# Kernel optimization log

Hardware: AMD Instinct MI355X
Metric: run time of the kernel (lower is better)

## Reference

```python
import jax, jax.numpy as jnp
import numpy as np

B, L, ENC, D, H, HD, MLP, R = 4, 512, 512, 1024, 16, 64, 4096, 32
NUM_BUCKETS, MAX_DISTANCE = 32, 128
EPS = 1e-6
NEG = -1e10


def rmsnorm(x, scale):
    var = jnp.mean(jnp.square(x), axis=-1, keepdims=True)
    return x * jax.lax.rsqrt(var + EPS) * scale


def rel_pos_bias(table, qlen, klen):
    # T5 causal (bidirectional=False) relative position bucketing.
    ctx = jnp.arange(qlen)[:, None]
    mem = jnp.arange(klen)[None, :]
    rp = mem - ctx                      # [q, k]
    n = -jnp.minimum(rp, 0)             # distance into the past
    max_exact = NUM_BUCKETS // 2
    is_small = n < max_exact
    large = max_exact + (
        jnp.log(jnp.maximum(n, 1).astype(jnp.float32) / max_exact)
        / np.log(MAX_DISTANCE / max_exact) * (NUM_BUCKETS - max_exact)
    ).astype(jnp.int32)
    large = jnp.minimum(large, NUM_BUCKETS - 1)
    bucket = jnp.where(is_small, n, large)
    return table[bucket].transpose(2, 0, 1)[None]  # [1, h, q, k]


def lora_dense(x, W, a, b):
    # x:[B,L,d]  W:[d,e]  a:[B,d,r]  b:[B,r,e]  -> xW + (xa)b per example
    out = jnp.einsum('bld,de->ble', x, W)
    low = jnp.einsum('bld,bdr->blr', x, a)
    return out + jnp.einsum('blr,bre->ble', low, b)


def attention(xq, xkv, Wq, Wk, Wv, Wo, qa, qb, ka, kb, va, vb, oa, ob, bias):
    b, ql, _ = xq.shape
    kl = xkv.shape[1]
    q = lora_dense(xq, Wq, qa, qb).reshape(b, ql, H, HD) * (1.0 / np.sqrt(HD))
    k = lora_dense(xkv, Wk, ka, kb).reshape(b, kl, H, HD)
    v = lora_dense(xkv, Wv, va, vb).reshape(b, kl, H, HD)
    scores = jnp.einsum('bqhd,bkhd->bhqk', q, k)
    if bias is not None:
        scores = scores + bias
    probs = jax.nn.softmax(scores, axis=-1)
    ctx = jnp.einsum('bhqk,bkhd->bqhd', probs, v).reshape(b, ql, H * HD)
    return lora_dense(ctx, Wo, oa, ob)


def setup_inputs() -> dict:
    key = jax.random.key(0)
    ks = jax.random.split(key, 32)
    s = 0.02
    inp = {
        'inputs':  jax.random.normal(ks[0], (B, L, D), jnp.float32),
        'encoded': jax.random.normal(ks[1], (B, ENC, D), jnp.float32),
        'lora_qa': jax.random.normal(ks[2], (B, 2, D, R), jnp.float32) * s,
        'lora_qb': jax.random.normal(ks[3], (B, 2, R, D), jnp.float32) * s,
        'lora_ka': jax.random.normal(ks[4], (B, 2, D, R), jnp.float32) * s,
        'lora_kb': jax.random.normal(ks[5], (B, 2, R, D), jnp.float32) * s,
        'lora_va': jax.random.normal(ks[6], (B, 2, D, R), jnp.float32) * s,
        'lora_vb': jax.random.normal(ks[7], (B, 2, R, D), jnp.float32) * s,
        'lora_oa': jax.random.normal(ks[8], (B, 2, D, R), jnp.float32) * s,
        'lora_ob': jax.random.normal(ks[9], (B, 2, R, D), jnp.float32) * s,
        'rel_table': jax.random.normal(ks[10], (NUM_BUCKETS, H), jnp.float32) * s,
        'ln1': jnp.ones((D,), jnp.float32),
        'ln2': jnp.ones((D,), jnp.float32),
        'ln3': jnp.ones((D,), jnp.float32),
        'sWq': jax.random.normal(ks[11], (D, H * HD), jnp.float32) * s,
        'sWk': jax.random.normal(ks[12], (D, H * HD), jnp.float32) * s,
        'sWv': jax.random.normal(ks[13], (D, H * HD), jnp.float32) * s,
        'sWo': jax.random.normal(ks[14], (H * HD, D), jnp.float32) * s,
        'cWq': jax.random.normal(ks[15], (D, H * HD), jnp.float32) * s,
        'cWk': jax.random.normal(ks[16], (D, H * HD), jnp.float32) * s,
        'cWv': jax.random.normal(ks[17], (D, H * HD), jnp.float32) * s,
        'cWo': jax.random.normal(ks[18], (H * HD, D), jnp.float32) * s,
        'wi0': jax.random.normal(ks[19], (D, MLP), jnp.float32) * s,
        'wi1': jax.random.normal(ks[20], (D, MLP), jnp.float32) * s,
        'wo_mlp': jax.random.normal(ks[21], (MLP, D), jnp.float32) * s,
    }
    return inp


def reference(inputs, encoded, lora_qa, lora_qb, lora_ka, lora_kb, lora_va, lora_vb,
              lora_oa, lora_ob, rel_table, ln1, ln2, ln3,
              sWq, sWk, sWv, sWo, cWq, cWk, cWv, cWo, wi0, wi1, wo_mlp):
    l = inputs.shape[1]
    causal = jnp.tril(jnp.ones((l, l), dtype=bool))
    dec_bias = rel_pos_bias(rel_table, l, l) + jnp.where(causal, 0.0, NEG)[None, None]

    # --- self-attention block ---
    x = rmsnorm(inputs, ln1)
    x = attention(x, x, sWq, sWk, sWv, sWo,
                  lora_qa[:, 0], lora_qb[:, 0], lora_ka[:, 0], lora_kb[:, 0],
                  lora_va[:, 0], lora_vb[:, 0], lora_oa[:, 0], lora_ob[:, 0],
                  dec_bias)
    x = x + inputs

    # --- cross-attention block ---
    y = rmsnorm(x, ln2)
    y = attention(y, encoded, cWq, cWk, cWv, cWo,
                  lora_qa[:, 1], lora_qb[:, 1], lora_ka[:, 1], lora_kb[:, 1],
                  lora_va[:, 1], lora_vb[:, 1], lora_oa[:, 1], lora_ob[:, 1],
                  None)
    y = y + x

    # --- gated-gelu MLP block (T5 v1.1 style) ---
    lz = rmsnorm(y, ln3)
    h = jax.nn.gelu(lz @ wi0, approximate=False) * (lz @ wi1)
    z = h @ wo_mlp + y
    return z
```

## Files before the change

### kernel.cpp

```cpp
#include <hip/hip_runtime.h>
#include <math.h>


#define DEV __device__ __forceinline__

typedef __bf16 bf16x8 __attribute__((ext_vector_type(8)));
typedef float floatx4 __attribute__((ext_vector_type(4)));

typedef __attribute__((address_space(1))) void* gas_ptr;
typedef __attribute__((address_space(3))) void* las_ptr;

DEV unsigned short f2bf(float f) {
  union { float f; unsigned int u; } v; v.f = f;
  unsigned int r = v.u + 0x7fffu + ((v.u >> 16) & 1u);
  return (unsigned short)(r >> 16);
}
DEV float bf2f(unsigned short u) {
  union { unsigned int u; float f; } v; v.u = ((unsigned int)u) << 16;
  return v.f;
}

#define GLOAD_LDS16(g, l) __builtin_amdgcn_global_load_lds((gas_ptr)(g), (las_ptr)(l), 16, 0, 0)

template<int NW>
DEV void stage_tile_sw(const char* gbase, char* lds, int nrows, int ldbytes, int wave, int lane) {
  int nchunks = nrows >> 3;
  int colb = (((lane & 7) ^ ((lane >> 3) & 7)) << 4);
  for (int c = wave; c < nchunks; c += NW) {
    int row = (c << 3) + (lane >> 3);
    GLOAD_LDS16(gbase + (size_t)row * ldbytes + colb, lds + (c << 10));
  }
}

template<int NW>
DEV void stage_tile256_sw(const char* gbase, char* lds, int nrows, int ldbytes, int wave, int lane) {
  int nchunks = nrows >> 2;
  for (int c = wave; c < nchunks; c += NW) {
    int row = (c << 2) + (lane >> 4);
    int key = row & 7;
    int colb = ((lane & 15) ^ key) << 4;
    GLOAD_LDS16(gbase + (size_t)row * ldbytes + colb, lds + (c << 10));
  }
}

template<int WM, int WN>
DEV void gemm_core(const unsigned short* A, const unsigned short* Bt, float* C,
                   int K, int lda, int ldb, int ldc, int m0, int n0,
                   char* ldsA, char* ldsB) {
  constexpr int NW = WM * WN;
  const int tid  = threadIdx.x;
  const int lane = tid & 63;
  const int wave = tid >> 6;
  const int wm   = wave % WM;
  const int wn   = wave / WM;
  const int quad = lane >> 4;
  const int l15  = lane & 15;
  const int key  = l15 & 7;

  floatx4 acc[4][4];
#pragma unroll
  for (int i = 0; i < 4; ++i)
#pragma unroll
    for (int j = 0; j < 4; ++j) acc[i][j] = (floatx4){0.f, 0.f, 0.f, 0.f};

  const char* gA = (const char*)(A + (size_t)m0 * lda);
  const char* gB = (const char*)(Bt + (size_t)n0 * ldb);

  for (int k0 = 0; k0 < K; k0 += 64) {
    stage_tile_sw<NW>(gA + (size_t)k0 * 2, ldsA, WM * 64, lda * 2, wave, lane);
    stage_tile_sw<NW>(gB + (size_t)k0 * 2, ldsB, WN * 64, ldb * 2, wave, lane);
    __syncthreads();
#pragma unroll
    for (int kk = 0; kk < 64; kk += 32) {
      bf16x8 af[4], bv[4];
      int off = (((kk >> 3) + quad) ^ key) << 4;
      const char* baseA = ldsA + (size_t)(wm * 64 + l15) * 128 + off;
      const char* baseB = ldsB + (size_t)(wn * 64 + l15) * 128 + off;
#pragma unroll
      for (int mi = 0; mi < 4; ++mi) af[mi] = *(const bf16x8*)(baseA + mi * 2048);
#pragma unroll
      for (int ni = 0; ni < 4; ++ni) bv[ni] = *(const bf16x8*)(baseB + ni * 2048);
#pragma unroll
      for (int mi = 0; mi < 4; ++mi)
#pragma unroll
        for (int ni = 0; ni < 4; ++ni)
          acc[mi][ni] = __builtin_amdgcn_mfma_f32_16x16x32_bf16(af[mi], bv[ni], acc[mi][ni], 0, 0, 0);
    }
    __syncthreads();
  }

#pragma unroll
  for (int mi = 0; mi < 4; ++mi) {
#pragma unroll
    for (int r = 0; r < 4; ++r) {
      int row = m0 + wm * 64 + mi * 16 + quad * 4 + r;
#pragma unroll
      for (int ni = 0; ni < 4; ++ni) {
        int col = n0 + wn * 64 + ni * 16 + l15;
        C[(size_t)row * ldc + col] = acc[mi][ni][r];
      }
    }
  }
}

__global__ __launch_bounds__(256) void k_gemm1s(const unsigned short* A, const unsigned short* Bt,
                                                float* Cpart, size_t pstride,
                                                int Kchunk, int lda, int ldb, int ldc) {
  __shared__ char lds[32768];
  int s = blockIdx.z;
  size_t koff = (size_t)s * Kchunk;
  gemm_core<2, 2>(A + koff, Bt + koff, Cpart + (size_t)s * pstride,
                  Kchunk, lda, ldb, ldc,
                  blockIdx.y * 128, blockIdx.x * 128, lds, lds + 16384);
}

struct GXSlice {
  const unsigned short* A0;
  const unsigned short* Aext;
  const unsigned short* B0;
  const unsigned short* Bext;
  float* C;
  size_t bextb;
  int ldc, nxa, it0, it1;
};
struct GX { GXSlice s[4]; };

__global__ __launch_bounds__(256) void k_gemmx(GX g) {
  __shared__ char lds[32768];
  char* ldsA = lds;
  char* ldsB = lds + 16384;
  GXSlice sl = g.s[blockIdx.z];
  if ((int)blockIdx.x >= sl.nxa) return;
  const int m0 = blockIdx.y * 128, n0 = blockIdx.x * 128;
  const int b = m0 >> 9;
  const int tid = threadIdx.x, lane = tid & 63, wave = tid >> 6;
  const int wm = wave & 1, wn = wave >> 1;
  const int quad = lane >> 4, l15 = lane & 15;
  const int key = l15 & 7;

  floatx4 acc[4][4];
#pragma unroll
  for (int i = 0; i < 4; ++i)
#pragma unroll
    for (int j = 0; j < 4; ++j) acc[i][j] = (floatx4){0.f, 0.f, 0.f, 0.f};

  for (int it = sl.it0; it < sl.it1; ++it) {
    if (it < 16) {
      stage_tile_sw<4>((const char*)sl.A0 + (size_t)m0 * 2048 + it * 128, ldsA, 128, 2048, wave, lane);
      stage_tile_sw<4>((const char*)sl.B0 + (size_t)n0 * 2048 + it * 128, ldsB, 128, 2048, wave, lane);
    } else {
      int eb = (it - 16) * 128;
      stage_tile_sw<4>((const char*)sl.Aext + (size_t)m0 * 256 + eb, ldsA, 128, 256, wave, lane);
      stage_tile_sw<4>((const char*)(sl.Bext + (size_t)b * sl.bextb) + (size_t)n0 * 256 + eb,
                       ldsB, 128, 256, wave, lane);
    }
    __syncthreads();
#pragma unroll
    for (int kk = 0; kk < 64; kk += 32) {
      bf16x8 af[4], bv[4];
      int off = (((kk >> 3) + quad) ^ key) << 4;
      const char* baseA = ldsA + (size_t)(wm * 64 + l15) * 128 + off;
      const char* baseB = ldsB + (size_t)(wn * 64 + l15) * 128 + off;
#pragma unroll
      for (int mi = 0; mi < 4; ++mi) af[mi] = *(const bf16x8*)(baseA + mi * 2048);
#pragma unroll
      for (int ni = 0; ni < 4; ++ni) bv[ni] = *(const bf16x8*)(baseB + ni * 2048);
#pragma unroll
      for (int mi = 0; mi < 4; ++mi)
#pragma unroll
        for (int ni = 0; ni < 4; ++ni)
          acc[mi][ni] = __builtin_amdgcn_mfma_f32_16x16x32_bf16(af[mi], bv[ni], acc[mi][ni], 0, 0, 0);
    }
    __syncthreads();
  }

#pragma unroll
  for (int mi = 0; mi < 4; ++mi) {
#pragma unroll
    for (int r = 0; r < 4; ++r) {
      int row = m0 + wm * 64 + mi * 16 + quad * 4 + r;
#pragma unroll
      for (int ni = 0; ni < 4; ++ni) {
        int col = n0 + wn * 64 + ni * 16 + l15;
        sl.C[(size_t)row * sl.ldc + col] = acc[mi][ni][r];
      }
    }
  }
}

struct QKVSlice {
  const unsigned short* A0;
  const unsigned short* Aext;
  const unsigned short* B0;
  const unsigned short* Bext;
  unsigned short* sec0;
  unsigned short* sec1;
  unsigned short* sec2;
  size_t bextb;
  int vsec, nxa;
};
struct QKV2 { QKVSlice s[2]; };

__global__ __launch_bounds__(256) void k_gemmqkv(QKV2 g) {
  __shared__ char lds[34816];
  char* ldsA = lds;
  char* ldsB = lds + 16384;
  QKVSlice sl = g.s[blockIdx.z];
  if ((int)blockIdx.x >= sl.nxa) return;
  const int m0 = blockIdx.y * 128, n0 = blockIdx.x * 128;
  const int b = m0 >> 9;
  const int tid = threadIdx.x, lane = tid & 63, wave = tid >> 6;
  const int wm = wave & 1, wn = wave >> 1;
  const int quad = lane >> 4, l15 = lane & 15;
  const int key = l15 & 7;

  floatx4 acc[4][4];
#pragma unroll
  for (int i = 0; i < 4; ++i)
#pragma unroll
    for (int j = 0; j < 4; ++j) acc[i][j] = (floatx4){0.f, 0.f, 0.f, 0.f};

  for (int it = 0; it < 18; ++it) {
    if (it < 16) {
      stage_tile_sw<4>((const char*)sl.A0 + (size_t)m0 * 2048 + it * 128, ldsA, 128, 2048, wave, lane);
      stage_tile_sw<4>((const char*)sl.B0 + (size_t)n0 * 2048 + it * 128, ldsB, 128, 2048, wave, lane);
    } else {
      int eb = (it - 16) * 128;
      stage_tile_sw<4>((const char*)sl.Aext + (size_t)m0 * 256 + eb, ldsA, 128, 256, wave, lane);
      stage_tile_sw<4>((const char*)(sl.Bext + (size_t)b * sl.bextb) + (size_t)n0 * 256 + eb,
                       ldsB, 128, 256, wave, lane);
    }
    __syncthreads();
#pragma unroll
    for (int kk = 0; kk < 64; kk += 32) {
      bf16x8 af[4], bv[4];
      int off = (((kk >> 3) + quad) ^ key) << 4;
      const char* baseA = ldsA + (size_t)(wm * 64 + l15) * 128 + off;
      const char* baseB = ldsB + (size_t)(wn * 64 + l15) * 128 + off;
#pragma unroll
      for (int mi = 0; mi < 4; ++mi) af[mi] = *(const bf16x8*)(baseA + mi * 2048);
#pragma unroll
      for (int ni = 0; ni < 4; ++ni) bv[ni] = *(const bf16x8*)(baseB + ni * 2048);
#pragma unroll
      for (int mi = 0; mi < 4; ++mi)
#pragma unroll
        for (int ni = 0; ni < 4; ++ni)
          acc[mi][ni] = __builtin_amdgcn_mfma_f32_16x16x32_bf16(af[mi], bv[ni], acc[mi][ni], 0, 0, 0);
    }
    __syncthreads();
  }

  const int sec = n0 >> 10;
  const int nloc = n0 & 1023;
  if (sec != sl.vsec) {
    unsigned short* dst = (sec == 0) ? sl.sec0 : sl.sec1;
#pragma unroll
    for (int mi = 0; mi < 4; ++mi)
#pragma unroll
      for (int r = 0; r < 4; ++r) {
        int row = m0 + wm * 64 + mi * 16 + quad * 4 + r;
        unsigned short* drow = dst + (size_t)row * 1024 + nloc + wn * 64;
#pragma unroll
        for (int ni = 0; ni < 4; ++ni)
          drow[ni * 16 + l15] = f2bf(acc[mi][ni][r]);
      }
  } else {
    unsigned short* vdstb = (sl.vsec == 1) ? sl.sec1 : sl.sec2;
    char* vbuf = lds + (size_t)(wm * 2 + wn) * 8704;
#pragma unroll
    for (int ni = 0; ni < 4; ++ni)
#pragma unroll
      for (int mi = 0; mi < 4; ++mi) {
        unsigned long long pk =
            (unsigned long long)f2bf(acc[mi][ni][0])
          | ((unsigned long long)f2bf(acc[mi][ni][1]) << 16)
          | ((unsigned long long)f2bf(acc[mi][ni][2]) << 32)
          | ((unsigned long long)f2bf(acc[mi][ni][3]) << 48);
        *(unsigned long long*)(vbuf + (size_t)(ni * 16 + l15) * 136 + (mi * 16 + quad * 4) * 2) = pk;
      }
    __syncthreads();
    int dbase = nloc + wn * 64;
    int h = dbase >> 6;
    int kb = (m0 & 511) + wm * 64;
    unsigned short* vdst = vdstb + (size_t)(b * 16 + h) * 64 * 512;
    int lh = lane >> 3, ll = lane & 7;
#pragma unroll
    for (int i = 0; i < 8; ++i) {
      int d = i * 8 + lh;
      const char* p = vbuf + (size_t)d * 136 + ll * 16;
      unsigned long long lo = *(const unsigned long long*)p;
      unsigned long long hi = *(const unsigned long long*)(p + 8);
      uint4 v;
      v.x = (unsigned)lo; v.y = (unsigned)(lo >> 32);
      v.z = (unsigned)hi; v.w = (unsigned)(hi >> 32);
      *(uint4*)(vdst + (size_t)d * 512 + kb + ll * 8) = v;
    }
  }
}

template<bool CAUSAL, bool QSUM>
__global__ __launch_bounds__(256) void k_flash(const unsigned short* qmat, const float* qparts,
                                               const unsigned short* kmat, const unsigned short* vt,
                                               const float* rb, unsigned short* ctxb) {
  __shared__ char ldsQ[8192];
  __shared__ char ldsK[16384];
  __shared__ char ldsV[16384];
  __shared__ char ldsP[16384];
  __shared__ float lrb[512];

  const size_t PART = (size_t)2048 * 1024;
  const int z = blockIdx.y, b = z >> 4, h = z & 15;
  const int q0 = blockIdx.x * 64;
  const int tid = threadIdx.x, lane = tid & 63, wave = tid >> 6;
  const int quad = lane >> 4, l15 = lane & 15;
  const int key = l15 & 7;

  const unsigned short* K = kmat + (size_t)b * 512 * 1024 + h * 64;
  const unsigned short* V = vt + (size_t)z * 64 * 512;

  if (QSUM) {
#pragma unroll
    for (int rr = 0; rr < 4; ++rr) {
      int row = rr * 16 + (tid >> 4);
      int c4 = tid & 15;
      const float* src = qparts + (size_t)(q0 + row) * 1024 + h * 64 + c4 * 4;
      float4 s0 = *(const float4*)src;
      float4 s1 = *(const float4*)(src + PART);
      float4 s2 = *(const float4*)(src + 2 * PART);
      float4 s3 = *(const float4*)(src + 3 * PART);
      ushort4 o;
      o.x = f2bf(s0.x + s1.x + s2.x + s3.x);
      o.y = f2bf(s0.y + s1.y + s2.y + s3.y);
      o.z = f2bf(s0.z + s1.z + s2.z + s3.z);
      o.w = f2bf(s0.w + s1.w + s2.w + s3.w);
      int qoff = (((c4 >> 1) ^ (row & 7)) << 4) | ((c4 & 1) << 3);
      *(ushort4*)(ldsQ + (size_t)row * 128 + qoff) = o;
    }
  } else {
    const unsigned short* Q = qmat + (size_t)b * 512 * 1024 + h * 64;
    stage_tile_sw<4>((const char*)(Q + (size_t)q0 * 1024), ldsQ, 64, 2048, wave, lane);
  }
  if (CAUSAL)
    for (int i = tid; i < 512; i += 256) lrb[i] = rb[h * 512 + i];

  float m_run[4], l_run[4];
  floatx4 oacc[4];
#pragma unroll
  for (int r = 0; r < 4; ++r) { m_run[r] = -1e30f; l_run[r] = 0.f; }
#pragma unroll
  for (int ni = 0; ni < 4; ++ni) oacc[ni] = (floatx4){0.f, 0.f, 0.f, 0.f};

  const int ktend = CAUSAL ? (blockIdx.x / 2 + 1) : 4;
  for (int kt = 0; kt < ktend; ++kt) {
    __syncthreads();
    stage_tile_sw<4>((const char*)(K + (size_t)kt * 128 * 1024), ldsK, 128, 2048, wave, lane);
    stage_tile256_sw<4>((const char*)(V + kt * 128), ldsV, 64, 1024, wave, lane);
    __syncthreads();

    floatx4 sacc[8];
#pragma unroll
    for (int ct = 0; ct < 8; ++ct) sacc[ct] = (floatx4){0.f, 0.f, 0.f, 0.f};
    const size_t qrow = (size_t)(wave * 16 + l15) * 128;
#pragma unroll
    for (int kd = 0; kd < 2; ++kd) {
      int offq = ((quad + kd * 4) ^ key) << 4;
      bf16x8 af = *(const bf16x8*)(ldsQ + qrow + offq);
#pragma unroll
      for (int ct = 0; ct < 8; ++ct) {
        bf16x8 bfv = *(const bf16x8*)(ldsK + (size_t)(ct * 16 + l15) * 128 + offq);
        sacc[ct] = __builtin_amdgcn_mfma_f32_16x16x32_bf16(af, bfv, sacc[ct], 0, 0, 0);
      }
    }

    float sv[8][4];
#pragma unroll
    for (int ct = 0; ct < 8; ++ct)
#pragma unroll
      for (int r = 0; r < 4; ++r) {
        float v = sacc[ct][r] * 0.125f;
        if (CAUSAL) {
          int qq = q0 + wave * 16 + quad * 4 + r;
          int kk = kt * 128 + ct * 16 + l15;
          v = (kk <= qq) ? v + lrb[qq - kk] : -1e30f;
        }
        sv[ct][r] = v;
      }

    float mx[4];
#pragma unroll
    for (int r = 0; r < 4; ++r) {
      mx[r] = sv[0][r];
#pragma unroll
      for (int ct = 1; ct < 8; ++ct) mx[r] = fmaxf(mx[r], sv[ct][r]);
    }
#pragma unroll
    for (int o = 1; o < 16; o <<= 1)
#pragma unroll
      for (int r = 0; r < 4; ++r) mx[r] = fmaxf(mx[r], __shfl_xor(mx[r], o));

    float alpha[4], rs[4];
#pragma unroll
    for (int r = 0; r < 4; ++r) {
      float mn = fmaxf(m_run[r], mx[r]);
      alpha[r] = __expf(m_run[r] - mn);
      m_run[r] = mn;
      rs[r] = 0.f;
    }
#pragma unroll
    for (int ct = 0; ct < 8; ++ct)
#pragma unroll
      for (int r = 0; r < 4; ++r) {
        float p = __expf(sv[ct][r] - m_run[r]);
        sv[ct][r] = p;
        rs[r] += p;
      }
#pragma unroll
    for (int o = 1; o < 16; o <<= 1)
#pragma unroll
      for (int r = 0; r < 4; ++r) rs[r] += __shfl_xor(rs[r], o);
#pragma unroll
    for (int r = 0; r < 4; ++r) l_run[r] = l_run[r] * alpha[r] + rs[r];
#pragma unroll
    for (int ni = 0; ni < 4; ++ni)
#pragma unroll
      for (int r = 0; r < 4; ++r) oacc[ni][r] *= alpha[r];

#pragma unroll
    for (int ct = 0; ct < 8; ++ct)
#pragma unroll
      for (int r = 0; r < 4; ++r) {
        int prow_w = wave * 16 + quad * 4 + r;
        int kidx = ct * 16 + l15;
        int pb = (((kidx >> 3) ^ (prow_w & 7)) << 4) | ((kidx & 7) << 1);
        *(unsigned short*)(ldsP + (size_t)prow_w * 256 + pb) = f2bf(sv[ct][r]);
      }
    __syncthreads();

    const size_t prow = (size_t)(wave * 16 + l15) * 256;
#pragma unroll
    for (int kk = 0; kk < 4; ++kk) {
      int offp = ((quad + kk * 4) ^ key) << 4;
      bf16x8 pf = *(const bf16x8*)(ldsP + prow + offp);
#pragma unroll
      for (int ni = 0; ni < 4; ++ni) {
        bf16x8 vf8 = *(const bf16x8*)(ldsV + (size_t)(ni * 16 + l15) * 256 + offp);
        oacc[ni] = __builtin_amdgcn_mfma_f32_16x16x32_bf16(pf, vf8, oacc[ni], 0, 0, 0);
      }
    }
  }

#pragma unroll
  for (int r = 0; r < 4; ++r) {
    int q = q0 + wave * 16 + quad * 4 + r;
    float inv = 1.0f / l_run[r];
    unsigned short* dst = ctxb + ((size_t)b * 512 + q) * 1024 + h * 64;
#pragma unroll
    for (int ni = 0; ni < 4; ++ni)
      dst[ni * 16 + l15] = f2bf(oacc[ni][r] * inv);
  }
}

__global__ __launch_bounds__(512) void k_mlp(const unsigned short* A, const unsigned short* Wc,
                                             unsigned short* hbf) {
  __shared__ char lds[49152];
  char* ldsA = lds;
  char* ldsB = lds + 16384;
  const int m0 = blockIdx.y * 128;
  const int n0 = blockIdx.x * 128;
  const int tid = threadIdx.x, lane = tid & 63, wave = tid >> 6;
  const int half = wave >> 2, wl = wave & 3;
  const int wm = wl & 1, wn = wl >> 1;
  const int quad = lane >> 4, l15 = lane & 15;
  const int key = l15 & 7;

  floatx4 acc[4][4];
#pragma unroll
  for (int i = 0; i < 4; ++i)
#pragma unroll
    for (int j = 0; j < 4; ++j) acc[i][j] = (floatx4){0.f, 0.f, 0.f, 0.f};

  const char* gA = (const char*)(A + (size_t)m0 * 1024);
  const char* gB = (const char*)(Wc + (size_t)blockIdx.x * 256 * 1024);

  for (int k0 = 0; k0 < 1024; k0 += 64) {
    stage_tile_sw<8>(gA + (size_t)k0 * 2, ldsA, 128, 2048, wave, lane);
    stage_tile_sw<8>(gB + (size_t)k0 * 2, ldsB, 256, 2048, wave, lane);
    __syncthreads();
#pragma unroll
    for (int kk = 0; kk < 64; kk += 32) {
      bf16x8 af[4], bv[4];
      int off = (((kk >> 3) + quad) ^ key) << 4;
      const char* baseA = ldsA + (size_t)(wm * 64 + l15) * 128 + off;
      const char* baseB = ldsB + (size_t)(half * 128 + wn * 64 + l15) * 128 + off;
#pragma unroll
      for (int mi = 0; mi < 4; ++mi) af[mi] = *(const bf16x8*)(baseA + mi * 2048);
#pragma unroll
      for (int ni = 0; ni < 4; ++ni) bv[ni] = *(const bf16x8*)(baseB + ni * 2048);
#pragma unroll
      for (int mi = 0; mi < 4; ++mi)
#pragma unroll
        for (int ni = 0; ni < 4; ++ni)
          acc[mi][ni] = __builtin_amdgcn_mfma_f32_16x16x32_bf16(af[mi], bv[ni], acc[mi][ni], 0, 0, 0);
    }
    __syncthreads();
  }

  if (half == 1) {
#pragma unroll
    for (int mi = 0; mi < 4; ++mi)
#pragma unroll
      for (int r = 0; r < 4; ++r) {
        int row = wm * 64 + mi * 16 + quad * 4 + r;
#pragma unroll
        for (int ni = 0; ni < 4; ++ni) {
          int col = wn * 64 + ni * 16 + l15;
          *(unsigned short*)(ldsB + (size_t)row * 256 + col * 2) = f2bf(acc[mi][ni][r]);
        }
      }
  }
  __syncthreads();
  if (half == 0) {
#pragma unroll
    for (int mi = 0; mi < 4; ++mi)
#pragma unroll
      for (int r = 0; r < 4; ++r) {
        int row = wm * 64 + mi * 16 + quad * 4 + r;
#pragma unroll
        for (int ni = 0; ni < 4; ++ni) {
          int col = wn * 64 + ni * 16 + l15;
          float h1 = bf2f(*(const unsigned short*)(ldsB + (size_t)row * 256 + col * 2));
          float g = acc[mi][ni][r];
          float v = 0.5f * g * (1.0f + erff(g * 0.70710678f)) * h1;
          hbf[(size_t)(m0 + row) * 4096 + n0 + col] = f2bf(v);
        }
      }
  }
}

struct PrepArgs {
  const float* src[11];
  unsigned short* dst[11];
  int K[11], N[11], mode[11];
  int tstart[12];
  const float* encoded;
  unsigned short* encbf;
  const float* table;
  float* rb;
  unsigned short* bmdst[5];
  const float* bmsrc[5][3];
  int bmnrg[5];
  int bmstart[6];
  int nwt, nf2bf, nbm;
};
__global__ __launch_bounds__(256, 2) void k_prep(PrepArgs a) {
  __shared__ float tl[64][65];
  int bid = blockIdx.x;
  int t = threadIdx.x;
  if (bid < a.nwt) {
    int z = 0;
    while (z < 10 && bid >= a.tstart[z + 1]) ++z;
    int tile = bid - a.tstart[z];
    int N = a.N[z], K = a.K[z], mode = a.mode[z];
    int ntn = N >> 6;
    int tn = tile % ntn, tk = tile / ntn;
    const float* src = a.src[z] + (size_t)(tk * 64) * N + tn * 64;
    unsigned short* dst = a.dst[z];
    {
      int rq = t >> 4, c4 = (t & 15) * 4;
      float4 v[4];
#pragma unroll
      for (int i = 0; i < 4; ++i)
        v[i] = *(const float4*)(src + (size_t)(rq + i * 16) * N + c4);
#pragma unroll
      for (int i = 0; i < 4; ++i) {
        int r = rq + i * 16;
        tl[r][c4] = v[i].x; tl[r][c4 + 1] = v[i].y;
        tl[r][c4 + 2] = v[i].z; tl[r][c4 + 3] = v[i].w;
      }
    }
    __syncthreads();
    {
      int nl = t >> 2, kseg = (t & 3) * 16;
      int n = tn * 64 + nl;
      int orow = (mode == 0) ? n : ((n >> 7) * 256 + ((mode == 2) ? 128 : 0) + (n & 127));
      union { unsigned short us[16]; uint4 q[2]; } pk;
#pragma unroll
      for (int j = 0; j < 16; ++j) pk.us[j] = f2bf(tl[kseg + j][nl]);
      uint4* dp = (uint4*)(dst + (size_t)orow * K + tk * 64 + kseg);
      dp[0] = pk.q[0]; dp[1] = pk.q[1];
    }
    return;
  }
  bid -= a.nwt;
  if (bid < a.nf2bf) {
    const float4* src = (const float4*)a.encoded;
    ushort4* dst = (ushort4*)a.encbf;
    int base = bid * 2048 + t;
    float4 v[8];
#pragma unroll
    for (int i = 0; i < 8; ++i) v[i] = src[base + i * 256];
#pragma unroll
    for (int i = 0; i < 8; ++i) {
      ushort4 o;
      o.x = f2bf(v[i].x); o.y = f2bf(v[i].y); o.z = f2bf(v[i].z); o.w = f2bf(v[i].w);
      dst[base + i * 256] = o;
    }
    return;
  }
  bid -= a.nf2bf;
  if (bid < 32) {
    int i = bid * 256 + t;
    if (i < 16 * 512) {
      int h = i >> 9, d = i & 511;
      int bucket;
      if (d < 16) bucket = d;
      else {
        int lb = 16 + (int)(logf((float)d / 16.0f) / logf(8.0f) * 16.0f);
        bucket = lb < 31 ? lb : 31;
      }
      a.rb[i] = a.table[bucket * 16 + h];
    }
    return;
  }
  bid -= 32;
  {
    int m = 0;
    while (m < 4 && bid >= a.bmstart[m + 1]) ++m;
    int idx = bid - a.bmstart[m];
    int nrg = a.bmnrg[m];
    int b = idx / nrg, rg = idx % nrg;
    int n0 = rg * 128;
    int sec = n0 >> 10;
    const float* src = a.bmsrc[m][sec] + (size_t)b * 65536;
    unsigned short* dst = a.bmdst[m] + ((size_t)b * nrg * 128 + n0) * 128;
    int n = t & 127, coff = (t >> 7) * 64;
    int ncol = (n0 & 1023) + n;
    unsigned short* drow = dst + (size_t)n * 128 + coff;
    for (int cg = 0; cg < 16; cg += 8) {
      float vv[8][4];
#pragma unroll
      for (int cc = 0; cc < 8; ++cc)
#pragma unroll
        for (int e = 0; e < 4; ++e) {
          int c = coff + (cg + cc) * 4 + e;
          vv[cc][e] = ((c >> 5) == sec) ? src[(size_t)(c & 31) * 1024 + ncol] : 0.f;
        }
#pragma unroll
      for (int cc = 0; cc < 8; ++cc) {
        ushort4 o;
        o.x = f2bf(vv[cc][0]); o.y = f2bf(vv[cc][1]);
        o.z = f2bf(vv[cc][2]); o.w = f2bf(vv[cc][3]);
        *(ushort4*)(drow + (cg + cc) * 4) = o;
      }
    }
  }
}

__global__ __launch_bounds__(256) void k_lowc(const float* encoded, const float* a0g,
                                              const float* a1g, unsigned short* lowc) {
  __shared__ float rowsF[8 * 1024];
  __shared__ float pacc[2 * 8 * 8 * 32];
  int t = threadIdx.x;
  int row0 = blockIdx.x * 8;
  int b = row0 >> 9;
  for (int j = 0; j < 8; ++j)
    ((float4*)(rowsF + j * 1024))[t] = ((const float4*)(encoded + (size_t)(row0 + j) * 1024))[t];
  __syncthreads();
  int r = t & 31, g = t >> 5;
  float acc[2][8];
#pragma unroll
  for (int p = 0; p < 2; ++p)
#pragma unroll
    for (int j = 0; j < 8; ++j) acc[p][j] = 0.f;
  const float* a0 = a0g + (size_t)b * 65536;
  const float* a1 = a1g + (size_t)b * 65536;
  for (int i = 0; i < 128; ++i) {
    int k = g * 128 + i;
    float ak = a0[(size_t)k * 32 + r];
    float av = a1[(size_t)k * 32 + r];
#pragma unroll
    for (int j = 0; j < 8; ++j) {
      float x = rowsF[j * 1024 + k];
      acc[0][j] += x * ak;
      acc[1][j] += x * av;
    }
  }
#pragma unroll
  for (int p = 0; p < 2; ++p)
#pragma unroll
    for (int j = 0; j < 8; ++j)
      pacc[((p * 8 + j) * 8 + g) * 32 + r] = acc[p][j];
  __syncthreads();
  for (int j = 0; j < 8; ++j) {
    if (t < 64) {
      int p = t >> 5, r2 = t & 31;
      float s = 0.f;
      for (int gg = 0; gg < 8; ++gg) s += pacc[((p * 8 + j) * 8 + gg) * 32 + r2];
      lowc[(size_t)(row0 + j) * 128 + p * 32 + r2] = f2bf(s);
    } else if (t < 128) {
      lowc[(size_t)(row0 + j) * 128 + t] = 0;
    }
  }
}

__global__ __launch_bounds__(256) void k_start(const float* x, const float* sc,
                                               const float* qa, const float* ka, const float* va,
                                               unsigned short* xn, unsigned short* lowext) {
  __shared__ unsigned short lrows[8][1024];
  __shared__ float pacc[3 * 8 * 8 * 32];
  __shared__ float red[4];
  int t = threadIdx.x;
  int row0 = blockIdx.x * 8;
  int b = row0 >> 9;
  float4 s4 = ((const float4*)sc)[t];
  for (int j = 0; j < 8; ++j) {
    int row = row0 + j;
    float4 v = ((const float4*)(x + (size_t)row * 1024))[t];
    float ss = v.x * v.x + v.y * v.y + v.z * v.z + v.w * v.w;
    for (int o = 32; o; o >>= 1) ss += __shfl_down(ss, o);
    if ((t & 63) == 0) red[t >> 6] = ss;
    __syncthreads();
    float tot = red[0] + red[1] + red[2] + red[3];
    float rs = rsqrtf(tot * (1.0f / 1024.0f) + 1e-6f);
    ushort4 o;
    o.x = f2bf(v.x * rs * s4.x); o.y = f2bf(v.y * rs * s4.y);
    o.z = f2bf(v.z * rs * s4.z); o.w = f2bf(v.w * rs * s4.w);
    ((ushort4*)(xn + (size_t)row * 1024))[t] = o;
    *(ushort4*)(&lrows[j][t * 4]) = o;
    __syncthreads();
  }
  int r = t & 31, g = t >> 5;
  float acc[3][8];
#pragma unroll
  for (int p = 0; p < 3; ++p)
#pragma unroll
    for (int j = 0; j < 8; ++j) acc[p][j] = 0.f;
  const float* aq = qa + (size_t)b * 65536;
  const float* ak = ka + (size_t)b * 65536;
  const float* av = va + (size_t)b * 65536;
  for (int i = 0; i < 128; ++i) {
    int k = g * 128 + i;
    float a0 = aq[(size_t)k * 32 + r];
    float a1 = ak[(size_t)k * 32 + r];
    float a2 = av[(size_t)k * 32 + r];
#pragma unroll
    for (int j = 0; j < 8; ++j) {
      float xv = bf2f(lrows[j][k]);
      acc[0][j] += xv * a0;
      acc[1][j] += xv * a1;
      acc[2][j] += xv * a2;
    }
  }
#pragma unroll
  for (int p = 0; p < 3; ++p)
#pragma unroll
    for (int j = 0; j < 8; ++j)
      pacc[((p * 8 + j) * 8 + g) * 32 + r] = acc[p][j];
  __syncthreads();
  for (int j = 0; j < 8; ++j) {
    if (t < 96) {
      int p = t >> 5, r2 = t & 31;
      float s = 0.f;
      for (int gg = 0; gg < 8; ++gg) s += pacc[((p * 8 + j) * 8 + gg) * 32 + r2];
      lowext[(size_t)(row0 + j) * 128 + p * 32 + r2] = f2bf(s);
    } else if (t < 128) {
      lowext[(size_t)(row0 + j) * 128 + t] = 0;
    }
  }
}

template<bool LOW>
__global__ __launch_bounds__(256) void k_addbrms(const float* parts, const float* resid,
                                                 const float* sc, float* resout,
                                                 unsigned short* xn,
                                                 const float* aP, unsigned short* lowext) {
  __shared__ unsigned short lrows[8][1024];
  __shared__ float pacc[8 * 8 * 32];
  __shared__ float red[4];
  const size_t PART = (size_t)2048 * 1024;
  int t = threadIdx.x;
  int row0 = blockIdx.x * 8;
  int b = row0 >> 9;
  float4 s4 = ((const float4*)sc)[t];
  for (int j = 0; j < 8; ++j) {
    int row = row0 + j;
    const float* p0 = parts + (size_t)row * 1024;
    float4 v = ((const float4*)p0)[t];
    float4 v1 = ((const float4*)(p0 + PART))[t];
    float4 v2 = ((const float4*)(p0 + 2 * PART))[t];
    float4 v3 = ((const float4*)(p0 + 3 * PART))[t];
    float4 rv = ((const float4*)(resid + (size_t)row * 1024))[t];
    float4 s;
    s.x = v.x + v1.x + v2.x + v3.x + rv.x;
    s.y = v.y + v1.y + v2.y + v3.y + rv.y;
    s.z = v.z + v1.z + v2.z + v3.z + rv.z;
    s.w = v.w + v1.w + v2.w + v3.w + rv.w;
    ((float4*)(resout + (size_t)row * 1024))[t] = s;
    float ss = s.x * s.x + s.y * s.y + s.z * s.z + s.w * s.w;
    for (int o = 32; o; o >>= 1) ss += __shfl_down(ss, o);
    if ((t & 63) == 0) red[t >> 6] = ss;
    __syncthreads();
    float tot = red[0] + red[1] + red[2] + red[3];
    float rs = rsqrtf(tot * (1.0f / 1024.0f) + 1e-6f);
    ushort4 o;
    o.x = f2bf(s.x * rs * s4.x); o.y = f2bf(s.y * rs * s4.y);
    o.z = f2bf(s.z * rs * s4.z); o.w = f2bf(s.w * rs * s4.w);
    ((ushort4*)(xn + (size_t)row * 1024))[t] = o;
    if (LOW) *(ushort4*)(&lrows[j][t * 4]) = o;
    __syncthreads();
  }
  if (LOW) {
    int r = t & 31, g = t >> 5;
    float acc[8];
#pragma unroll
    for (int j = 0; j < 8; ++j) acc[j] = 0.f;
    const float* ap = aP + (size_t)b * 65536;
    for (int i = 0; i < 128; ++i) {
      int k = g * 128 + i;
      float a0 = ap[(size_t)k * 32 + r];
#pragma unroll
      for (int j = 0; j < 8; ++j) acc[j] += bf2f(lrows[j][k]) * a0;
    }
#pragma unroll
    for (int j = 0; j < 8; ++j) pacc[(j * 8 + g) * 32 + r] = acc[j];
    __syncthreads();
    for (int j = 0; j < 8; ++j) {
      if (t < 32) {
        float s = 0.f;
        for (int gg = 0; gg < 8; ++gg) s += pacc[(j * 8 + gg) * 32 + t];
        lowext[(size_t)(row0 + j) * 128 + t] = f2bf(s);
      } else if (t < 128) {
        lowext[(size_t)(row0 + j) * 128 + t] = 0;
      }
    }
  }
}

__global__ __launch_bounds__(256) void k_lowbf(const unsigned short* x, const float* a,
                                               unsigned short* lowext) {
  int row0 = blockIdx.x * 8;
  int b = row0 >> 9;
  int t = threadIdx.x, r = t & 31, j = t >> 5;
  int row = row0 + j;
  const bf16x8* xv = (const bf16x8*)(x + (size_t)row * 1024);
  const float* ap = a + (size_t)b * 65536;
  float s = 0.f;
  for (int kb = 0; kb < 128; ++kb) {
    bf16x8 v = xv[kb];
#pragma unroll
    for (int u = 0; u < 8; ++u)
      s += (float)v[u] * ap[(size_t)(kb * 8 + u) * 32 + r];
  }
  lowext[(size_t)row * 128 + r] = f2bf(s);
  lowext[(size_t)row * 128 + 32 + r] = 0;
  lowext[(size_t)row * 128 + 64 + r] = 0;
  lowext[(size_t)row * 128 + 96 + r] = 0;
}

__global__ void k_sum4(const float* p, size_t pstride, const float* resid, float* out) {
  int i = blockIdx.x * 256 + threadIdx.x;
  float4 a = ((const float4*)p)[i];
  float4 b = ((const float4*)(p + pstride))[i];
  float4 c = ((const float4*)(p + 2 * pstride))[i];
  float4 d = ((const float4*)(p + 3 * pstride))[i];
  float4 r = ((const float4*)resid)[i];
  float4 o;
  o.x = a.x + b.x + c.x + d.x + r.x;
  o.y = a.y + b.y + c.y + d.y + r.y;
  o.z = a.z + b.z + c.z + d.z + r.z;
  o.w = a.w + b.w + c.w + d.w + r.w;
  ((float4*)out)[i] = o;
}


extern "C" void kernel_launch(void* const* d_in, const int* in_sizes, int n_in,
                              void* d_out, int out_size, void* d_ws, size_t ws_size,
                              hipStream_t stream) {
  const float* f_inputs  = (const float*)d_in[0];
  const float* f_encoded = (const float*)d_in[1];
  const float* f_qa = (const float*)d_in[2];
  const float* f_qb = (const float*)d_in[3];
  const float* f_ka = (const float*)d_in[4];
  const float* f_kb = (const float*)d_in[5];
  const float* f_va = (const float*)d_in[6];
  const float* f_vb = (const float*)d_in[7];
  const float* f_oa = (const float*)d_in[8];
  const float* f_ob = (const float*)d_in[9];
  const float* f_table = (const float*)d_in[10];
  const float* f_ln1 = (const float*)d_in[11];
  const float* f_ln2 = (const float*)d_in[12];
  const float* f_ln3 = (const float*)d_in[13];
  const float* f_W[8] = { (const float*)d_in[14], (const float*)d_in[15],
                          (const float*)d_in[16], (const float*)d_in[17],
                          (const float*)d_in[18], (const float*)d_in[19],
                          (const float*)d_in[20], (const float*)d_in[21] };
  const float* f_wi0 = (const float*)d_in[22];
  const float* f_wi1 = (const float*)d_in[23];
  const float* f_wo  = (const float*)d_in[24];

  const size_t SEL1 = 32768;
  const size_t PART = (size_t)2048 * 1024;

  char* w = (char*)d_ws;
  size_t off = 0;
  auto alloc = [&](size_t bytes) -> char* {
    off = (off + 255) & ~(size_t)255;
    char* p = w + off;
    off += bytes;
    return p;
  };
  unsigned short* wt  = (unsigned short*)alloc((size_t)8192 * 1024 * 2);
  unsigned short* wc  = (unsigned short*)alloc((size_t)8192 * 1024 * 2);
  unsigned short* wot = (unsigned short*)alloc((size_t)1024 * 4096 * 2);
  unsigned short* encbf = (unsigned short*)alloc(2048 * 1024 * 2);
  float* rb = (float*)alloc(16 * 512 * 4);
  unsigned short* xn  = (unsigned short*)alloc(2048 * 1024 * 2);
  unsigned short* qbf = (unsigned short*)alloc(2048 * 1024 * 2);
  unsigned short* kbf = (unsigned short*)alloc(2048 * 1024 * 2);
  unsigned short* vtb = (unsigned short*)alloc((size_t)64 * 64 * 512 * 2);
  unsigned short* kbf2 = (unsigned short*)alloc(2048 * 1024 * 2);
  unsigned short* vtb2 = (unsigned short*)alloc((size_t)64 * 64 * 512 * 2);
  unsigned short* lowext_s = (unsigned short*)alloc(2048 * 128 * 2);
  unsigned short* lowext_c = (unsigned short*)alloc(2048 * 128 * 2);
  unsigned short* lowext_q = (unsigned short*)alloc(2048 * 128 * 2);
  unsigned short* lowext_o = (unsigned short*)alloc(2048 * 128 * 2);
  unsigned short* bmext_s  = (unsigned short*)alloc((size_t)4 * 3072 * 128 * 2);
  unsigned short* bmext_c  = (unsigned short*)alloc((size_t)4 * 2048 * 128 * 2);
  unsigned short* bmext_q  = (unsigned short*)alloc((size_t)4 * 1024 * 128 * 2);
  unsigned short* bmext_o  = (unsigned short*)alloc((size_t)4 * 1024 * 128 * 2);
  unsigned short* bmext_o2 = (unsigned short*)alloc((size_t)4 * 1024 * 128 * 2);
  unsigned short* ctxb = (unsigned short*)alloc(2048 * 1024 * 2);
  float* xres = (float*)alloc(2048 * 1024 * 4);
  float* yres = (float*)alloc(2048 * 1024 * 4);
  char*  big  = alloc((size_t)84 << 20);
  float* op_s = (float*)big;
  float* qp_c = (float*)(big + ((size_t)32 << 20));
  float* op_c = (float*)big;
  unsigned short* hbf = (unsigned short*)big;
  float* fp   = (float*)(big + ((size_t)16 << 20));
  (void)ws_size; (void)in_sizes; (void)n_in; (void)out_size;

  PrepArgs pa;
  int ts = 0;
  for (int i = 0; i < 8; ++i) {
    pa.src[i] = f_W[i]; pa.dst[i] = wt + (size_t)i * 1024 * 1024;
    pa.K[i] = 1024; pa.N[i] = 1024; pa.mode[i] = 0;
    pa.tstart[i] = ts; ts += 256;
  }
  pa.src[8] = f_wi0; pa.dst[8] = wc; pa.K[8] = 1024; pa.N[8] = 4096; pa.mode[8] = 1;
  pa.tstart[8] = ts; ts += 1024;
  pa.src[9] = f_wi1; pa.dst[9] = wc; pa.K[9] = 1024; pa.N[9] = 4096; pa.mode[9] = 2;
  pa.tstart[9] = ts; ts += 1024;
  pa.src[10] = f_wo; pa.dst[10] = wot; pa.K[10] = 4096; pa.N[10] = 1024; pa.mode[10] = 0;
  pa.tstart[10] = ts; ts += 1024;
  pa.tstart[11] = ts;
  pa.nwt = ts;
  pa.encoded = f_encoded; pa.encbf = encbf;
  pa.table = f_table; pa.rb = rb;
  pa.nf2bf = 256;
  pa.bmdst[0] = bmext_s;  pa.bmnrg[0] = 24;
  pa.bmsrc[0][0] = f_qb; pa.bmsrc[0][1] = f_kb; pa.bmsrc[0][2] = f_vb;
  pa.bmdst[1] = bmext_c;  pa.bmnrg[1] = 16;
  pa.bmsrc[1][0] = f_kb + SEL1; pa.bmsrc[1][1] = f_vb + SEL1; pa.bmsrc[1][2] = nullptr;
  pa.bmdst[2] = bmext_q;  pa.bmnrg[2] = 8;
  pa.bmsrc[2][0] = f_qb + SEL1; pa.bmsrc[2][1] = nullptr; pa.bmsrc[2][2] = nullptr;
  pa.bmdst[3] = bmext_o;  pa.bmnrg[3] = 8;
  pa.bmsrc[3][0] = f_ob; pa.bmsrc[3][1] = nullptr; pa.bmsrc[3][2] = nullptr;
  pa.bmdst[4] = bmext_o2; pa.bmnrg[4] = 8;
  pa.bmsrc[4][0] = f_ob + SEL1; pa.bmsrc[4][1] = nullptr; pa.bmsrc[4][2] = nullptr;
  int bs = 0;
  for (int m = 0; m < 5; ++m) { pa.bmstart[m] = bs; bs += pa.bmnrg[m] * 4; }
  pa.bmstart[5] = bs;
  pa.nbm = bs;
  int totblk = pa.nwt + pa.nf2bf + 32 + pa.nbm;
  k_prep<<<dim3(totblk), dim3(256), 0, stream>>>(pa);
  k_lowc<<<dim3(256), dim3(256), 0, stream>>>(f_encoded, f_ka + SEL1, f_va + SEL1, lowext_c);

  k_start<<<dim3(256), dim3(256), 0, stream>>>(f_inputs, f_ln1, f_qa, f_ka, f_va, xn, lowext_s);

  {
    QKV2 g;
    g.s[0] = { xn, lowext_s, wt, bmext_s,
               qbf, kbf, vtb, (size_t)3072 * 128, 2, 24 };
    g.s[1] = { encbf, lowext_c, wt + (size_t)5120 * 1024, bmext_c,
               kbf2, vtb2, nullptr, (size_t)2048 * 128, 1, 16 };
    k_gemmqkv<<<dim3(24, 16, 2), dim3(256), 0, stream>>>(g);
  }

  k_flash<true, false><<<dim3(8, 64), dim3(256), 0, stream>>>(qbf, nullptr, kbf, vtb, rb, ctxb);

  k_lowbf<<<dim3(256), dim3(256), 0, stream>>>(ctxb, f_oa, lowext_o);
  {
    GX g;
    for (int s = 0; s < 4; ++s)
      g.s[s] = { ctxb, lowext_o, wt + (size_t)3072 * 1024, bmext_o, op_s + (size_t)s * PART,
                 (size_t)1024 * 128, 1024, 8, s * 18 / 4, (s + 1) * 18 / 4 };
    k_gemmx<<<dim3(8, 16, 4), dim3(256), 0, stream>>>(g);
  }
  k_addbrms<true><<<dim3(256), dim3(256), 0, stream>>>(op_s, f_inputs, f_ln2, xres, xn,
                                                       f_qa + SEL1, lowext_q);

  {
    GX g;
    for (int s = 0; s < 4; ++s)
      g.s[s] = { xn, lowext_q, wt + (size_t)4096 * 1024, bmext_q, qp_c + (size_t)s * PART,
                 (size_t)1024 * 128, 1024, 8, s * 18 / 4, (s + 1) * 18 / 4 };
    k_gemmx<<<dim3(8, 16, 4), dim3(256), 0, stream>>>(g);
  }
  k_flash<false, true><<<dim3(8, 64), dim3(256), 0, stream>>>(nullptr, qp_c, kbf2, vtb2, rb, ctxb);

  k_lowbf<<<dim3(256), dim3(256), 0, stream>>>(ctxb, f_oa + SEL1, lowext_o);
  {
    GX g;
    for (int s = 0; s < 4; ++s)
      g.s[s] = { ctxb, lowext_o, wt + (size_t)7168 * 1024, bmext_o2, op_c + (size_t)s * PART,
                 (size_t)1024 * 128, 1024, 8, s * 18 / 4, (s + 1) * 18 / 4 };
    k_gemmx<<<dim3(8, 16, 4), dim3(256), 0, stream>>>(g);
  }
  k_addbrms<false><<<dim3(256), dim3(256), 0, stream>>>(op_c, xres, f_ln3, yres, xn,
                                                        nullptr, nullptr);

  k_mlp<<<dim3(32, 16), dim3(512), 0, stream>>>(xn, wc, hbf);
  k_gemm1s<<<dim3(8, 16, 4), dim3(256), 0, stream>>>(hbf, wot, fp, PART, 1024, 4096, 4096, 1024);
  k_sum4<<<dim3(2048), dim3(256), 0, stream>>>(fp, PART, yres, (float*)d_out);
}
```

Before: 549.5 us.

## Fuse cross-attn Q projection into bf16 qkv GEMM and batch weight-prep tiles

The cross-attention Q projection now goes through the qkv GEMM kernel, which writes bf16 Q directly. This replaces a 4-way split-K fp32 partial GEMM whose four partials the flash kernel had to sum. That removes the fp32 partial traffic and the reduction inside flash, but the GEMM grid shrinks from 512 blocks to 128 with no split-K, which may underfill the GPU. Separately, the weight transpose/convert prep kernel now handles two 64x64 tiles per block with both loads issued up front, halving its block count.

```diff
diff --git a/kernel.cpp b/kernel.cpp
--- a/kernel.cpp
+++ b/kernel.cpp
@@ -559,34 +559,39 @@
   if (bid < a.nwt) {
     int z = 0;
     while (z < 10 && bid >= a.tstart[z + 1]) ++z;
-    int tile = bid - a.tstart[z];
+    int pair = bid - a.tstart[z];
     int N = a.N[z], K = a.K[z], mode = a.mode[z];
     int ntn = N >> 6;
-    int tn = tile % ntn, tk = tile / ntn;
-    const float* src = a.src[z] + (size_t)(tk * 64) * N + tn * 64;
-    unsigned short* dst = a.dst[z];
-    {
-      int rq = t >> 4, c4 = (t & 15) * 4;
-      float4 v[4];
+    int rq = t >> 4, c4 = (t & 15) * 4;
+    float4 v[2][4];
+#pragma unroll
+    for (int rep = 0; rep < 2; ++rep) {
+      int tile = pair * 2 + rep;
+      int tn = tile % ntn, tk = tile / ntn;
+      const float* src = a.src[z] + (size_t)(tk * 64) * N + tn * 64;
 #pragma unroll
       for (int i = 0; i < 4; ++i)
-        v[i] = *(const float4*)(src + (size_t)(rq + i * 16) * N + c4);
+        v[rep][i] = *(const float4*)(src + (size_t)(rq + i * 16) * N + c4);
+    }
+#pragma unroll
+    for (int rep = 0; rep < 2; ++rep) {
+      __syncthreads();
 #pragma unroll
       for (int i = 0; i < 4; ++i) {
         int r = rq + i * 16;
-        tl[r][c4] = v[i].x; tl[r][c4 + 1] = v[i].y;
-        tl[r][c4 + 2] = v[i].z; tl[r][c4 + 3] = v[i].w;
-      }
-    }
-    __syncthreads();
-    {
+        tl[r][c4] = v[rep][i].x; tl[r][c4 + 1] = v[rep][i].y;
+        tl[r][c4 + 2] = v[rep][i].z; tl[r][c4 + 3] = v[rep][i].w;
+      }
+      __syncthreads();
+      int tile = pair * 2 + rep;
+      int tn = tile % ntn, tk = tile / ntn;
       int nl = t >> 2, kseg = (t & 3) * 16;
       int n = tn * 64 + nl;
       int orow = (mode == 0) ? n : ((n >> 7) * 256 + ((mode == 2) ? 128 : 0) + (n & 127));
       union { unsigned short us[16]; uint4 q[2]; } pk;
 #pragma unroll
       for (int j = 0; j < 16; ++j) pk.us[j] = f2bf(tl[kseg + j][nl]);
-      uint4* dp = (uint4*)(dst + (size_t)orow * K + tk * 64 + kseg);
+      uint4* dp = (uint4*)(a.dst[z] + (size_t)orow * K + tk * 64 + kseg);
       dp[0] = pk.q[0]; dp[1] = pk.q[1];
     }
     return;
@@ -934,7 +939,6 @@
   float* yres = (float*)alloc(2048 * 1024 * 4);
   char*  big  = alloc((size_t)84 << 20);
   float* op_s = (float*)big;
-  float* qp_c = (float*)(big + ((size_t)32 << 20));
   float* op_c = (float*)big;
   unsigned short* hbf = (unsigned short*)big;
   float* fp   = (float*)(big + ((size_t)16 << 20));
@@ -945,14 +949,14 @@
   for (int i = 0; i < 8; ++i) {
     pa.src[i] = f_W[i]; pa.dst[i] = wt + (size_t)i * 1024 * 1024;
     pa.K[i] = 1024; pa.N[i] = 1024; pa.mode[i] = 0;
-    pa.tstart[i] = ts; ts += 256;
+    pa.tstart[i] = ts; ts += 128;
   }
   pa.src[8] = f_wi0; pa.dst[8] = wc; pa.K[8] = 1024; pa.N[8] = 4096; pa.mode[8] = 1;
-  pa.tstart[8] = ts; ts += 1024;
+  pa.tstart[8] = ts; ts += 512;
   pa.src[9] = f_wi1; pa.dst[9] = wc; pa.K[9] = 1024; pa.N[9] = 4096; pa.mode[9] = 2;
-  pa.tstart[9] = ts; ts += 1024;
+  pa.tstart[9] = ts; ts += 512;
   pa.src[10] = f_wo; pa.dst[10] = wot; pa.K[10] = 4096; pa.N[10] = 1024; pa.mode[10] = 0;
-  pa.tstart[10] = ts; ts += 1024;
+  pa.tstart[10] = ts; ts += 512;
   pa.tstart[11] = ts;
   pa.nwt = ts;
   pa.encoded = f_encoded; pa.encbf = encbf;
@@ -1001,13 +1005,13 @@
                                                        f_qa + SEL1, lowext_q);
 
   {
-    GX g;
-    for (int s = 0; s < 4; ++s)
-      g.s[s] = { xn, lowext_q, wt + (size_t)4096 * 1024, bmext_q, qp_c + (size_t)s * PART,
-                 (size_t)1024 * 128, 1024, 8, s * 18 / 4, (s + 1) * 18 / 4 };
-    k_gemmx<<<dim3(8, 16, 4), dim3(256), 0, stream>>>(g);
-  }
-  k_flash<false, true><<<dim3(8, 64), dim3(256), 0, stream>>>(nullptr, qp_c, kbf2, vtb2, rb, ctxb);
+    QKV2 g;
+    g.s[0] = { xn, lowext_q, wt + (size_t)4096 * 1024, bmext_q,
+               qbf, nullptr, nullptr, (size_t)1024 * 128, -1, 8 };
+    g.s[1] = g.s[0];
+    k_gemmqkv<<<dim3(8, 16, 1), dim3(256), 0, stream>>>(g);
+  }
+  k_flash<false, false><<<dim3(8, 64), dim3(256), 0, stream>>>(qbf, nullptr, kbf2, vtb2, rb, ctxb);
 
   k_lowbf<<<dim3(256), dim3(256), 0, stream>>>(ctxb, f_oa + SEL1, lowext_o);
   {
```

New measurement: 560.8 us. 2.1% more time.
